# Kernel tuning notes

Measured on AMD Instinct MI355X. Metric: run time of the kernel, lower is better.

Reference implementation:

```python
import jax, jax.numpy as jnp
import numpy as np
import math

B_SZ, L, D_MODEL = 2, 2048, 1024
D_STATE, D_CONV, EXPAND = 16, 4, 2
D_INNER = EXPAND * D_MODEL
DT_RANK = math.ceil(D_MODEL / 16)


def setup_inputs() -> dict:
    key = jax.random.key(0)
    ks = jax.random.split(key, 9)
    s = 0.02
    x = jax.random.normal(ks[0], (B_SZ, L, D_MODEL), jnp.float32)
    W_in = jax.random.normal(ks[1], (D_MODEL, 2 * D_INNER), jnp.float32) * s
    conv_w = jax.random.normal(ks[2], (D_INNER, D_CONV), jnp.float32) * 0.1
    conv_b = jax.random.normal(ks[3], (D_INNER,), jnp.float32) * s
    W_xproj = jax.random.normal(ks[4], (D_INNER, DT_RANK + 2 * D_STATE), jnp.float32) * s
    W_dt = jax.random.normal(ks[5], (DT_RANK, D_INNER), jnp.float32) * s
    # dt bias init so softplus(bias) is log-uniform in [dt_min, dt_max]
    dt_min, dt_max = 0.001, 0.1
    dt = jnp.exp(jax.random.uniform(ks[6], (D_INNER,)) * (math.log(dt_max) - math.log(dt_min)) + math.log(dt_min))
    dt = jnp.maximum(dt, 1e-4)
    b_dt = dt + jnp.log(-jnp.expm1(-dt))
    A_log = jnp.log(jnp.broadcast_to(jnp.arange(1, D_STATE + 1, dtype=jnp.float32), (D_INNER, D_STATE)))
    D = jnp.ones((D_INNER,), jnp.float32)
    W_out = jax.random.normal(ks[7], (D_INNER, D_MODEL), jnp.float32) * s
    return {"x": x, "W_in": W_in, "conv_w": conv_w, "conv_b": conv_b,
            "W_xproj": W_xproj, "W_dt": W_dt, "b_dt": b_dt,
            "A_log": A_log, "D": D, "W_out": W_out}


def _silu(v):
    return v * jax.nn.sigmoid(v)


def _mamba_fwd(x, W_in, conv_w, conv_b, W_xproj, W_dt, b_dt, A_log, D, W_out):
    B, Ls, _ = x.shape
    xz = x @ W_in                         # (B, L, 2*d_inner)
    xb, z = jnp.split(xz, 2, axis=-1)
    # causal depthwise conv1d (pad left d_conv-1, truncate to L)
    xp = jnp.pad(xb, ((0, 0), (D_CONV - 1, 0), (0, 0)))
    conv = conv_b
    acc = jnp.zeros_like(xb)
    for k in range(D_CONV):
        acc = acc + xp[:, k:k + Ls, :] * conv_w[:, k]
    xb = _silu(acc + conv_b)
    # input-dependent dt, B, C
    proj = xb @ W_xproj                   # (B, L, dt_rank + 2*d_state)
    dt_in = proj[..., :DT_RANK]
    Bm = proj[..., DT_RANK:DT_RANK + D_STATE]   # (B, L, d_state)
    Cm = proj[..., DT_RANK + D_STATE:]          # (B, L, d_state)
    dt = jax.nn.softplus(dt_in @ W_dt + b_dt)   # (B, L, d_inner)
    A = -jnp.exp(A_log)                         # (d_inner, d_state)

    def step(h, inp):
        x_t, dt_t, B_t, C_t = inp               # (B,d_inner),(B,d_inner),(B,s),(B,s)
        dA = jnp.exp(dt_t[:, :, None] * A)      # (B, d_inner, d_state)
        h = dA * h + (dt_t[:, :, None] * B_t[:, None, :]) * x_t[:, :, None]
        y_t = jnp.einsum('bds,bs->bd', h, C_t)
        return h, y_t

    h0 = jnp.zeros((B, D_INNER, D_STATE), xb.dtype)
    xs = (xb.swapaxes(0, 1), dt.swapaxes(0, 1), Bm.swapaxes(0, 1), Cm.swapaxes(0, 1))
    _, ys = jax.lax.scan(step, h0, xs)          # (L, B, d_inner)
    y = ys.swapaxes(0, 1) + D * xb
    y = y * _silu(z)
    return y @ W_out                            # (B, L, d_model)


def reference(x, W_in, conv_w, conv_b, W_xproj, W_dt, b_dt, A_log, D, W_out):
    return _mamba_fwd(x, W_in, conv_w, conv_b, W_xproj, W_dt, b_dt, A_log, D, W_out)
```

## Files before the change

### kernel.cpp

```cpp
#include <hip/hip_runtime.h>
#include <hip/hip_bf16.h>
#include <math.h>

#define BSZ 2
#define LSEQ 2048
#define DMODEL 1024
#define DSTATE 16
#define DCONV 4
#define DINNER 2048
#define DTRANK 64
#define NPROJ (DTRANK + 2 * DSTATE)
#define NC 32
#define LC 64
#define KS 4
#define KCH (DINNER / KS)
#define TT 8

using short8 = __attribute__((ext_vector_type(8))) short;
using f32x4 = __attribute__((ext_vector_type(4))) float;
using u16x4 = __attribute__((ext_vector_type(4))) unsigned short;

__device__ __forceinline__ float silu_f(float v) {
    return v / (1.f + expf(-v));
}
__device__ __forceinline__ float softplus_f(float v) {
    return fmaxf(v, 0.f) + log1pf(expf(-fabsf(v)));
}
__device__ __forceinline__ unsigned short f2bf(float f) {
    unsigned u = __builtin_bit_cast(unsigned, f);
    u += 0x7fffu + ((u >> 16) & 1u);
    return (unsigned short)(u >> 16);
}
__device__ __forceinline__ float bf2f(unsigned short u) {
    unsigned x = ((unsigned)u) << 16;
    return __builtin_bit_cast(float, x);
}

__device__ __forceinline__ void gld_lds16(const unsigned short* g, unsigned short* l) {
    __builtin_amdgcn_global_load_lds(
        (const __attribute__((address_space(1))) unsigned int*)g,
        (__attribute__((address_space(3))) unsigned int*)l, 16, 0, 0);
}

__global__ __launch_bounds__(256) void f32_to_bf16_kernel(
    const float* __restrict__ in, unsigned short* __restrict__ out, int n4) {
    int i = blockIdx.x * 256 + threadIdx.x;
    if (i >= n4) return;
    float4 v = reinterpret_cast<const float4*>(in)[i];
    u16x4 o = {f2bf(v.x), f2bf(v.y), f2bf(v.z), f2bf(v.w)};
    reinterpret_cast<u16x4*>(out)[i] = o;
}

__global__ __launch_bounds__(256) void transpose_bf16_kernel(
    const float* __restrict__ in, unsigned short* __restrict__ out, int R, int Cc) {
    __shared__ float t[32][33];
    const int tx = threadIdx.x & 31, ty = threadIdx.x >> 5;
    const int c0 = blockIdx.x * 32, r0 = blockIdx.y * 32;
    for (int i = ty; i < 32; i += 8)
        t[i][tx] = in[(size_t)(r0 + i) * Cc + c0 + tx];
    __syncthreads();
    for (int i = ty; i < 32; i += 8)
        out[(size_t)(c0 + i) * R + r0 + tx] = f2bf(t[tx][i]);
}

template <int EPI, typename CT>
__global__ __launch_bounds__(512) void gemm256(
    const unsigned short* __restrict__ A, const unsigned short* __restrict__ Bt,
    CT* __restrict__ C, CT* __restrict__ C2, int M, int N, int K) {
    extern __shared__ __align__(16) unsigned short lds[];
    unsigned short* As = lds;
    unsigned short* Bs = lds + 3 * 8192;
    const int tid = threadIdx.x;
    const int lane = tid & 63;
    const int w = tid >> 6;
    const int wm = w >> 2, wn = w & 3;
    const int m0 = blockIdx.y * 256, n0 = blockIdx.x * 256;
    const int fr = lane & 15, kg = lane >> 4;
    const int kswz = ((kg ^ ((fr >> 1) & 3)) << 3);
    const int srow = tid >> 2;
    const int cs8 = (((tid & 3) ^ ((tid >> 3) & 3)) << 3);
    const int dst = tid * 8;
    const int nt = K / 32;

    f32x4 acc[8][4];
#pragma unroll
    for (int m = 0; m < 8; m++)
#pragma unroll
        for (int n = 0; n < 4; n++) acc[m][n] = (f32x4){0.f, 0.f, 0.f, 0.f};

#define STAGE_A(t)                                                               \
    {                                                                            \
        const int _b = (t) % 3, _k = (t) * 32;                                   \
        gld_lds16(&A[(size_t)(m0 + srow) * K + _k + cs8], &As[_b * 8192 + dst]); \
        gld_lds16(&A[(size_t)(m0 + 128 + srow) * K + _k + cs8],                  \
                  &As[_b * 8192 + dst + 4096]);                                  \
    }
#define STAGE_B(t)                                                               \
    {                                                                            \
        const int _b = (t) % 3, _k = (t) * 32;                                   \
        gld_lds16(&Bt[(size_t)(n0 + srow) * K + _k + cs8], &Bs[_b * 8192 + dst]);\
        gld_lds16(&Bt[(size_t)(n0 + 128 + srow) * K + _k + cs8],                 \
                  &Bs[_b * 8192 + dst + 4096]);                                  \
    }

    STAGE_A(0); STAGE_B(0); STAGE_A(1); STAGE_B(1);
    asm volatile("s_waitcnt vmcnt(4)" ::: "memory");
    __builtin_amdgcn_s_barrier();

    short8 bfr[4];
    for (int t = 0; t < nt; t++) {
        const int buf = t % 3;
        short8 afr[4];
#pragma unroll
        for (int q = 0; q < 4; q++)
            afr[q] = *reinterpret_cast<const short8*>(
                &As[buf * 8192 + (wm * 128 + q * 16 + fr) * 32 + kswz]);
#pragma unroll
        for (int q = 0; q < 4; q++)
            bfr[q] = *reinterpret_cast<const short8*>(
                &Bs[buf * 8192 + (wn * 64 + q * 16 + fr) * 32 + kswz]);
        if (t + 2 < nt) STAGE_A(t + 2);
        __builtin_amdgcn_s_barrier();
        asm volatile("s_waitcnt lgkmcnt(0)" ::: "memory");
        __builtin_amdgcn_sched_barrier(0);
        __builtin_amdgcn_s_setprio(1);
#pragma unroll
        for (int m = 0; m < 4; m++)
#pragma unroll
            for (int n = 0; n < 4; n++)
                acc[m][n] = __builtin_amdgcn_mfma_f32_16x16x32_bf16(
                    afr[m], bfr[n], acc[m][n], 0, 0, 0);
        __builtin_amdgcn_s_setprio(0);
        __builtin_amdgcn_s_barrier();
#pragma unroll
        for (int q = 0; q < 4; q++)
            afr[q] = *reinterpret_cast<const short8*>(
                &As[buf * 8192 + (wm * 128 + 64 + q * 16 + fr) * 32 + kswz]);
        if (t + 2 < nt) STAGE_B(t + 2);
        if (t + 1 < nt) {
            if (t + 2 < nt)
                asm volatile("s_waitcnt vmcnt(4)" ::: "memory");
            else
                asm volatile("s_waitcnt vmcnt(0)" ::: "memory");
        }
        __builtin_amdgcn_s_barrier();
        asm volatile("s_waitcnt lgkmcnt(0)" ::: "memory");
        __builtin_amdgcn_sched_barrier(0);
        __builtin_amdgcn_s_setprio(1);
#pragma unroll
        for (int m = 0; m < 4; m++)
#pragma unroll
            for (int n = 0; n < 4; n++)
                acc[4 + m][n] = __builtin_amdgcn_mfma_f32_16x16x32_bf16(
                    afr[m], bfr[n], acc[4 + m][n], 0, 0, 0);
        __builtin_amdgcn_s_setprio(0);
        __builtin_amdgcn_s_barrier();
    }
#undef STAGE_A
#undef STAGE_B

    const int g4 = kg * 4;
#pragma unroll
    for (int m = 0; m < 8; m++)
#pragma unroll
        for (int n = 0; n < 4; n++)
#pragma unroll
            for (int j = 0; j < 4; j++) {
                int mm = m0 + wm * 128 + m * 16 + g4 + j;
                int nn = n0 + wn * 64 + n * 16 + fr;
                float v = acc[m][n][j];
                if (EPI == 1) {
                    if (nn < DINNER)
                        C[(size_t)mm * DINNER + nn] = f2bf(v);
                    else
                        C2[(size_t)mm * DINNER + (nn - DINNER)] = f2bf(silu_f(v));
                } else {
                    if constexpr (sizeof(CT) == 2)
                        C[(size_t)mm * N + nn] = f2bf(v);
                    else
                        C[(size_t)mm * N + nn] = v;
                }
            }
}

template <int EPI, int BN, typename CT>
__global__ __launch_bounds__(256) void gemm_mfma(
    const unsigned short* __restrict__ A, const unsigned short* __restrict__ Bt,
    CT* __restrict__ C, CT* __restrict__ C2, const float* __restrict__ bias,
    int M, int N, int K) {
    constexpr int NF = BN / 32;
    __shared__ __align__(16) unsigned short As[2][4096];
    __shared__ __align__(16) unsigned short Bs[2][BN * 32];
    const int tid = threadIdx.x;
    const int lane = tid & 63;
    const int wid = tid >> 6;
    const int wr = wid >> 1, wc = wid & 1;
    const int m0 = blockIdx.y * 128, n0 = blockIdx.x * BN;

    const int r0 = tid >> 2;
    const int r1 = r0 + 64;
    const int d0 = tid * 8;
    const int d1 = d0 + 2048;
    const int cs8 = (((tid & 3) ^ ((tid >> 3) & 3)) << 3);

    f32x4 acc[4][NF];
#pragma unroll
    for (int m = 0; m < 4; m++)
#pragma unroll
        for (int n = 0; n < NF; n++) acc[m][n] = (f32x4){0.f, 0.f, 0.f, 0.f};

    const int fr = lane & 15;
    const int kg = lane >> 4;
    const int kswz = ((kg ^ ((fr >> 1) & 3)) << 3);
    const int nt = K / 32;

    gld_lds16(&A[(size_t)(m0 + r0) * K + cs8], &As[0][d0]);
    gld_lds16(&A[(size_t)(m0 + r1) * K + cs8], &As[0][d1]);
    gld_lds16(&Bt[(size_t)(n0 + r0) * K + cs8], &Bs[0][d0]);
    if constexpr (BN == 128)
        gld_lds16(&Bt[(size_t)(n0 + r1) * K + cs8], &Bs[0][d1]);
    __syncthreads();

    int cur = 0;
    for (int t = 0; t < nt; t++) {
        if (t + 1 < nt) {
            const int k0 = (t + 1) * 32;
            gld_lds16(&A[(size_t)(m0 + r0) * K + k0 + cs8], &As[cur ^ 1][d0]);
            gld_lds16(&A[(size_t)(m0 + r1) * K + k0 + cs8], &As[cur ^ 1][d1]);
            gld_lds16(&Bt[(size_t)(n0 + r0) * K + k0 + cs8], &Bs[cur ^ 1][d0]);
            if constexpr (BN == 128)
                gld_lds16(&Bt[(size_t)(n0 + r1) * K + k0 + cs8], &Bs[cur ^ 1][d1]);
        }
        short8 a[4], b[NF];
#pragma unroll
        for (int m = 0; m < 4; m++)
            a[m] = *reinterpret_cast<const short8*>(
                &As[cur][(wr * 64 + m * 16 + fr) * 32 + kswz]);
#pragma unroll
        for (int n = 0; n < NF; n++)
            b[n] = *reinterpret_cast<const short8*>(
                &Bs[cur][(wc * (BN / 2) + n * 16 + fr) * 32 + kswz]);
#pragma unroll
        for (int m = 0; m < 4; m++)
#pragma unroll
            for (int n = 0; n < NF; n++)
                acc[m][n] = __builtin_amdgcn_mfma_f32_16x16x32_bf16(
                    a[m], b[n], acc[m][n], 0, 0, 0);
        __syncthreads();
        cur ^= 1;
    }

    const int g4 = (lane >> 4) * 4;
#pragma unroll
    for (int m = 0; m < 4; m++)
#pragma unroll
        for (int n = 0; n < NF; n++)
#pragma unroll
            for (int j = 0; j < 4; j++) {
                int mm = m0 + wr * 64 + m * 16 + g4 + j;
                int nn = n0 + wc * (BN / 2) + n * 16 + fr;
                float v = acc[m][n][j];
                if (EPI == 2) v = softplus_f(v + bias[nn]);
                if constexpr (sizeof(CT) == 2)
                    C[(size_t)mm * N + nn] = f2bf(v);
                else
                    C[(size_t)mm * N + nn] = v;
            }
}

__global__ __launch_bounds__(256) void proj_splitk(
    const unsigned short* __restrict__ Abf,
    const unsigned short* __restrict__ WxT,
    float* __restrict__ pp) {
    const int lane = threadIdx.x & 63;
    const int wid = threadIdx.x >> 6;
    const int mt = wid >> 1;
    const int nh = wid & 1;
    const int m0 = blockIdx.x * 32;
    const int kc = blockIdx.y;
    const int fr = lane & 15;
    const int kg = lane >> 4;

    const size_t abase = (size_t)(m0 + mt * 16 + fr) * DINNER + kc * KCH + kg * 8;

    f32x4 acc[3];
#pragma unroll
    for (int i = 0; i < 3; i++) acc[i] = (f32x4){0.f, 0.f, 0.f, 0.f};

    for (int step = 0; step < KCH / 32; step++) {
        short8 a = *reinterpret_cast<const short8*>(&Abf[abase + step * 32]);
#pragma unroll
        for (int nt = 0; nt < 3; nt++) {
            int nrow = nh * 48 + nt * 16 + fr;
            short8 b = *reinterpret_cast<const short8*>(
                &WxT[(size_t)nrow * DINNER + kc * KCH + step * 32 + kg * 8]);
            acc[nt] = __builtin_amdgcn_mfma_f32_16x16x32_bf16(a, b, acc[nt], 0, 0, 0);
        }
    }
    const int g4 = (lane >> 4) * 4;
#pragma unroll
    for (int nt = 0; nt < 3; nt++)
#pragma unroll
        for (int j = 0; j < 4; j++) {
            int m = m0 + mt * 16 + g4 + j;
            int n = nh * 48 + nt * 16 + fr;
            pp[((size_t)kc * (BSZ * LSEQ) + m) * NPROJ + n] = acc[nt][j];
        }
}

__global__ __launch_bounds__(256) void proj_reduce(
    const float* __restrict__ pp, float* __restrict__ proj,
    unsigned short* __restrict__ dtin) {
    int i = blockIdx.x * 256 + threadIdx.x;
    if (i >= BSZ * LSEQ * NPROJ) return;
    float s = 0.f;
#pragma unroll
    for (int kc = 0; kc < KS; kc++)
        s += pp[(size_t)kc * BSZ * LSEQ * NPROJ + i];
    proj[i] = s;
    int m = i / NPROJ;
    int n = i - m * NPROJ;
    if (n < DTRANK) dtin[(size_t)m * DTRANK + n] = f2bf(s);
}

__global__ __launch_bounds__(256) void conv_silu_kernel(
    const unsigned short* __restrict__ xin, const float* __restrict__ w,
    const float* __restrict__ bconv, unsigned short* __restrict__ xout) {
    const int tid = threadIdx.x;
    const int d0 = tid * 8;
    const int bt0 = blockIdx.x * TT;
    const int tloc = bt0 & (LSEQ - 1);

    float wk0[8], wk1[8], wk2[8], wk3[8], bb[8];
#pragma unroll
    for (int q = 0; q < 8; q++) {
        float4 wv = *reinterpret_cast<const float4*>(&w[(d0 + q) * 4]);
        wk0[q] = wv.x; wk1[q] = wv.y; wk2[q] = wv.z; wk3[q] = wv.w;
    }
    {
        float4 b0 = *reinterpret_cast<const float4*>(&bconv[d0]);
        float4 b1 = *reinterpret_cast<const float4*>(&bconv[d0 + 4]);
        bb[0] = b0.x; bb[1] = b0.y; bb[2] = b0.z; bb[3] = b0.w;
        bb[4] = b1.x; bb[5] = b1.y; bb[6] = b1.z; bb[7] = b1.w;
    }

    float xm3[8], xm2[8], xm1[8];
    if (tloc >= 3) {
        short8 v3 = *reinterpret_cast<const short8*>(&xin[(size_t)(bt0 - 3) * DINNER + d0]);
        short8 v2 = *reinterpret_cast<const short8*>(&xin[(size_t)(bt0 - 2) * DINNER + d0]);
        short8 v1 = *reinterpret_cast<const short8*>(&xin[(size_t)(bt0 - 1) * DINNER + d0]);
#pragma unroll
        for (int q = 0; q < 8; q++) {
            xm3[q] = bf2f((unsigned short)v3[q]);
            xm2[q] = bf2f((unsigned short)v2[q]);
            xm1[q] = bf2f((unsigned short)v1[q]);
        }
    } else {
#pragma unroll
        for (int q = 0; q < 8; q++) { xm3[q] = 0.f; xm2[q] = 0.f; xm1[q] = 0.f; }
    }

#pragma unroll
    for (int i = 0; i < TT; i++) {
        short8 vc = *reinterpret_cast<const short8*>(&xin[(size_t)(bt0 + i) * DINNER + d0]);
        float xc[8];
        short8 o;
#pragma unroll
        for (int q = 0; q < 8; q++) {
            xc[q] = bf2f((unsigned short)vc[q]);
            float a = bb[q];
            a = fmaf(wk0[q], xm3[q], a);
            a = fmaf(wk1[q], xm2[q], a);
            a = fmaf(wk2[q], xm1[q], a);
            a = fmaf(wk3[q], xc[q], a);
            o[q] = (short)f2bf(silu_f(a));
        }
        *reinterpret_cast<short8*>(&xout[(size_t)(bt0 + i) * DINNER + d0]) = o;
#pragma unroll
        for (int q = 0; q < 8; q++) { xm3[q] = xm2[q]; xm2[q] = xm1[q]; xm1[q] = xc[q]; }
    }
}

__global__ __launch_bounds__(256) void scan_pass1(
    const unsigned short* __restrict__ xb, const unsigned short* __restrict__ dt,
    const float* __restrict__ proj, const float* __restrict__ A_log,
    float* __restrict__ aprod, float* __restrict__ hend) {
    __shared__ float Bs[LC][DSTATE];
    const int tg = blockIdx.x * 256 + threadIdx.x;
    const int d = tg & (DINNER - 1);
    const int bc = tg >> 11;
    const int c = bc & (NC - 1);
    const int b = bc >> 5;

    for (int idx = threadIdx.x; idx < LC * DSTATE; idx += 256) {
        int ti = idx >> 4, j = idx & 15;
        Bs[ti][j] = proj[(size_t)(b * LSEQ + c * LC + ti) * NPROJ + DTRANK + j];
    }
    __syncthreads();

    float Av[DSTATE], h[DSTATE], ap[DSTATE];
#pragma unroll
    for (int s = 0; s < DSTATE; s++) {
        Av[s] = -expf(A_log[d * DSTATE + s]);
        h[s] = 0.f;
        ap[s] = 1.f;
    }

    for (int i = 0; i < LC; i++) {
        size_t base = (size_t)(b * LSEQ + c * LC + i) * DINNER + d;
        float dtv = bf2f(dt[base]);
        float xv = bf2f(xb[base]);
        float dx = dtv * xv;
#pragma unroll
        for (int s = 0; s < DSTATE; s++) {
            float dA = __expf(dtv * Av[s]);
            ap[s] *= dA;
            h[s] = fmaf(dA, h[s], dx * Bs[i][s]);
        }
    }

    size_t o = ((size_t)bc * DINNER + d) * DSTATE;
#pragma unroll
    for (int q = 0; q < 4; q++) {
        *reinterpret_cast<float4*>(&aprod[o + q * 4]) =
            make_float4(ap[4 * q], ap[4 * q + 1], ap[4 * q + 2], ap[4 * q + 3]);
        *reinterpret_cast<float4*>(&hend[o + q * 4]) =
            make_float4(h[4 * q], h[4 * q + 1], h[4 * q + 2], h[4 * q + 3]);
    }
}

__global__ __launch_bounds__(256) void scan_pass2(
    float* __restrict__ aprod, const float* __restrict__ hend) {
    const int tg = blockIdx.x * 256 + threadIdx.x;
    const int s = tg & (DSTATE - 1);
    const int d = (tg >> 4) & (DINNER - 1);
    const int b = tg >> 15;
    float h = 0.f;
    for (int c = 0; c < NC; c++) {
        size_t o = ((size_t)((b * NC + c) * DINNER) + d) * DSTATE + s;
        float a = aprod[o];
        float e = hend[o];
        aprod[o] = h;
        h = fmaf(a, h, e);
    }
}

__global__ __launch_bounds__(256) void scan_pass3(
    const unsigned short* __restrict__ xb, const unsigned short* __restrict__ dt,
    const float* __restrict__ proj, const float* __restrict__ hstart,
    const float* __restrict__ A_log, const float* __restrict__ Dp,
    const unsigned short* __restrict__ sz, unsigned short* __restrict__ ybf) {
    __shared__ float Bs[LC][DSTATE];
    __shared__ float Cs[LC][DSTATE];
    const int tg = blockIdx.x * 256 + threadIdx.x;
    const int d = tg & (DINNER - 1);
    const int bc = tg >> 11;
    const int c = bc & (NC - 1);
    const int b = bc >> 5;

    for (int idx = threadIdx.x; idx < LC * 2 * DSTATE; idx += 256) {
        int ti = idx >> 5, j = idx & 31;
        float v = proj[(size_t)(b * LSEQ + c * LC + ti) * NPROJ + DTRANK + j];
        if (j < DSTATE) Bs[ti][j] = v;
        else            Cs[ti][j - DSTATE] = v;
    }
    __syncthreads();

    float Av[DSTATE], h[DSTATE];
    size_t o = ((size_t)bc * DINNER + d) * DSTATE;
#pragma unroll
    for (int q = 0; q < 4; q++) {
        float4 hv = *reinterpret_cast<const float4*>(&hstart[o + q * 4]);
        h[4 * q] = hv.x; h[4 * q + 1] = hv.y; h[4 * q + 2] = hv.z; h[4 * q + 3] = hv.w;
    }
#pragma unroll
    for (int s = 0; s < DSTATE; s++)
        Av[s] = -expf(A_log[d * DSTATE + s]);
    const float Dd = Dp[d];

    for (int i = 0; i < LC; i++) {
        size_t base = (size_t)(b * LSEQ + c * LC + i) * DINNER + d;
        float dtv = bf2f(dt[base]);
        float xv = bf2f(xb[base]);
        float szv = bf2f(sz[base]);
        float dx = dtv * xv;
        float p = 0.f;
#pragma unroll
        for (int s = 0; s < DSTATE; s++) {
            float dA = __expf(dtv * Av[s]);
            h[s] = fmaf(dA, h[s], dx * Bs[i][s]);
            p = fmaf(h[s], Cs[i][s], p);
        }
        ybf[base] = f2bf((p + Dd * xv) * szv);
    }
}

extern "C" void kernel_launch(void* const* d_in, const int* in_sizes, int n_in,
                              void* d_out, int out_size, void* d_ws,
                              size_t ws_size, hipStream_t stream) {
    const float* x = (const float*)d_in[0];
    const float* W_in = (const float*)d_in[1];
    const float* conv_w = (const float*)d_in[2];
    const float* conv_b = (const float*)d_in[3];
    const float* W_xproj = (const float*)d_in[4];
    const float* W_dt = (const float*)d_in[5];
    const float* b_dt = (const float*)d_in[6];
    const float* A_log = (const float*)d_in[7];
    const float* Dp = (const float*)d_in[8];
    const float* W_out = (const float*)d_in[9];
    float* out = (float*)d_out;

    char* ws = (char*)d_ws;
    const size_t MB = 1u << 20;
    float* pp    = (float*)(ws);
    float* aprod = (float*)(ws);
    float* hend  = (float*)(ws + 8 * MB);
    unsigned short* xbpre_bf = (unsigned short*)(ws + 16 * MB);
    unsigned short* sz_bf    = (unsigned short*)(ws + 32 * MB);
    unsigned short* xb_bf    = (unsigned short*)(ws + 48 * MB);
    unsigned short* dt_bf    = (unsigned short*)(ws + 64 * MB);
    unsigned short* ybf      = (unsigned short*)(ws + 80 * MB);
    float* projbuf           = (float*)(ws + 88 * MB);
    unsigned short* dtin_bf  = (unsigned short*)(ws + 90 * MB);
    unsigned short* xbf      = (unsigned short*)(ws + 91 * MB);
    unsigned short* WinT     = (unsigned short*)(ws + 99 * MB);
    unsigned short* WoutT    = (unsigned short*)(ws + 107 * MB);
    unsigned short* WxT      = (unsigned short*)(ws + 111 * MB);
    unsigned short* WdtT     = (unsigned short*)(ws + 112 * MB);

    const int M = BSZ * LSEQ;
    dim3 blk(256);

    f32_to_bf16_kernel<<<dim3((M * DMODEL / 4 + 255) / 256), blk, 0, stream>>>(
        x, xbf, M * DMODEL / 4);
    transpose_bf16_kernel<<<dim3(2 * DINNER / 32, DMODEL / 32), blk, 0, stream>>>(
        W_in, WinT, DMODEL, 2 * DINNER);
    transpose_bf16_kernel<<<dim3(DMODEL / 32, DINNER / 32), blk, 0, stream>>>(
        W_out, WoutT, DINNER, DMODEL);
    transpose_bf16_kernel<<<dim3(NPROJ / 32, DINNER / 32), blk, 0, stream>>>(
        W_xproj, WxT, DINNER, NPROJ);
    transpose_bf16_kernel<<<dim3(DINNER / 32, DTRANK / 32), blk, 0, stream>>>(
        W_dt, WdtT, DTRANK, DINNER);

    gemm256<1, unsigned short><<<dim3((2 * DINNER) / 256, M / 256), dim3(512),
                                 98304, stream>>>(
        xbf, WinT, xbpre_bf, sz_bf, M, 2 * DINNER, DMODEL);

    conv_silu_kernel<<<dim3(M / TT), blk, 0, stream>>>(
        xbpre_bf, conv_w, conv_b, xb_bf);

    proj_splitk<<<dim3(M / 32, KS), blk, 0, stream>>>(xb_bf, WxT, pp);
    proj_reduce<<<dim3((M * NPROJ) / 256), blk, 0, stream>>>(pp, projbuf, dtin_bf);

    gemm_mfma<2, 128, unsigned short><<<dim3(DINNER / 128, M / 128), blk, 0, stream>>>(
        dtin_bf, WdtT, dt_bf, nullptr, b_dt, M, DINNER, DTRANK);

    const int nthreads1 = BSZ * NC * DINNER;
    scan_pass1<<<dim3(nthreads1 / 256), blk, 0, stream>>>(
        xb_bf, dt_bf, projbuf, A_log, aprod, hend);
    const int nthreads2 = BSZ * DINNER * DSTATE;
    scan_pass2<<<dim3(nthreads2 / 256), blk, 0, stream>>>(aprod, hend);
    scan_pass3<<<dim3(nthreads1 / 256), blk, 0, stream>>>(
        xb_bf, dt_bf, projbuf, aprod, A_log, Dp, sz_bf, ybf);

    gemm_mfma<0, 128, float><<<dim3(DMODEL / 128, M / 128), blk, 0, stream>>>(
        ybf, WoutT, out, nullptr, nullptr, M, DMODEL, DINNER);
}
```

Before: 274.6 us.

## Add XCD-aware block swizzle and dedicated LDS-free dt projection GEMM

```diff
diff --git a/kernel.cpp b/kernel.cpp
--- a/kernel.cpp
+++ b/kernel.cpp
@@ -42,6 +42,10 @@
         (__attribute__((address_space(3))) unsigned int*)l, 16, 0, 0);
 }
 
+__device__ __forceinline__ int xcd_swz(int wg, int nwg) {
+    return (wg & 7) * (nwg >> 3) + (wg >> 3);
+}
+
 __global__ __launch_bounds__(256) void f32_to_bf16_kernel(
     const float* __restrict__ in, unsigned short* __restrict__ out, int n4) {
     int i = blockIdx.x * 256 + threadIdx.x;
@@ -74,7 +78,9 @@
     const int lane = tid & 63;
     const int w = tid >> 6;
     const int wm = w >> 2, wn = w & 3;
-    const int m0 = blockIdx.y * 256, n0 = blockIdx.x * 256;
+    const int nwg = gridDim.x * gridDim.y;
+    const int wg = xcd_swz(blockIdx.y * gridDim.x + blockIdx.x, nwg);
+    const int m0 = (wg / gridDim.x) * 256, n0 = (wg % gridDim.x) * 256;
     const int fr = lane & 15, kg = lane >> 4;
     const int kswz = ((kg ^ ((fr >> 1) & 3)) << 3);
     const int srow = tid >> 2;
@@ -183,19 +189,19 @@
             }
 }
 
-template <int EPI, int BN, typename CT>
+template <int EPI, typename CT>
 __global__ __launch_bounds__(256) void gemm_mfma(
     const unsigned short* __restrict__ A, const unsigned short* __restrict__ Bt,
-    CT* __restrict__ C, CT* __restrict__ C2, const float* __restrict__ bias,
-    int M, int N, int K) {
-    constexpr int NF = BN / 32;
+    CT* __restrict__ C, int M, int N, int K) {
     __shared__ __align__(16) unsigned short As[2][4096];
-    __shared__ __align__(16) unsigned short Bs[2][BN * 32];
+    __shared__ __align__(16) unsigned short Bs[2][4096];
     const int tid = threadIdx.x;
     const int lane = tid & 63;
     const int wid = tid >> 6;
     const int wr = wid >> 1, wc = wid & 1;
-    const int m0 = blockIdx.y * 128, n0 = blockIdx.x * BN;
+    const int nwg = gridDim.x * gridDim.y;
+    const int wg = xcd_swz(blockIdx.y * gridDim.x + blockIdx.x, nwg);
+    const int m0 = (wg / gridDim.x) * 128, n0 = (wg % gridDim.x) * 128;
 
     const int r0 = tid >> 2;
     const int r1 = r0 + 64;
@@ -203,11 +209,11 @@
     const int d1 = d0 + 2048;
     const int cs8 = (((tid & 3) ^ ((tid >> 3) & 3)) << 3);
 
-    f32x4 acc[4][NF];
+    f32x4 acc[4][4];
 #pragma unroll
     for (int m = 0; m < 4; m++)
 #pragma unroll
-        for (int n = 0; n < NF; n++) acc[m][n] = (f32x4){0.f, 0.f, 0.f, 0.f};
+        for (int n = 0; n < 4; n++) acc[m][n] = (f32x4){0.f, 0.f, 0.f, 0.f};
 
     const int fr = lane & 15;
     const int kg = lane >> 4;
@@ -217,8 +223,7 @@
     gld_lds16(&A[(size_t)(m0 + r0) * K + cs8], &As[0][d0]);
     gld_lds16(&A[(size_t)(m0 + r1) * K + cs8], &As[0][d1]);
     gld_lds16(&Bt[(size_t)(n0 + r0) * K + cs8], &Bs[0][d0]);
-    if constexpr (BN == 128)
-        gld_lds16(&Bt[(size_t)(n0 + r1) * K + cs8], &Bs[0][d1]);
+    gld_lds16(&Bt[(size_t)(n0 + r1) * K + cs8], &Bs[0][d1]);
     __syncthreads();
 
     int cur = 0;
@@ -228,22 +233,21 @@
             gld_lds16(&A[(size_t)(m0 + r0) * K + k0 + cs8], &As[cur ^ 1][d0]);
             gld_lds16(&A[(size_t)(m0 + r1) * K + k0 + cs8], &As[cur ^ 1][d1]);
             gld_lds16(&Bt[(size_t)(n0 + r0) * K + k0 + cs8], &Bs[cur ^ 1][d0]);
-            if constexpr (BN == 128)
-                gld_lds16(&Bt[(size_t)(n0 + r1) * K + k0 + cs8], &Bs[cur ^ 1][d1]);
-        }
-        short8 a[4], b[NF];
+            gld_lds16(&Bt[(size_t)(n0 + r1) * K + k0 + cs8], &Bs[cur ^ 1][d1]);
+        }
+        short8 a[4], b[4];
 #pragma unroll
         for (int m = 0; m < 4; m++)
             a[m] = *reinterpret_cast<const short8*>(
                 &As[cur][(wr * 64 + m * 16 + fr) * 32 + kswz]);
 #pragma unroll
-        for (int n = 0; n < NF; n++)
+        for (int n = 0; n < 4; n++)
             b[n] = *reinterpret_cast<const short8*>(
-                &Bs[cur][(wc * (BN / 2) + n * 16 + fr) * 32 + kswz]);
+                &Bs[cur][(wc * 64 + n * 16 + fr) * 32 + kswz]);
 #pragma unroll
         for (int m = 0; m < 4; m++)
 #pragma unroll
-            for (int n = 0; n < NF; n++)
+            for (int n = 0; n < 4; n++)
                 acc[m][n] = __builtin_amdgcn_mfma_f32_16x16x32_bf16(
                     a[m], b[n], acc[m][n], 0, 0, 0);
         __syncthreads();
@@ -254,18 +258,55 @@
 #pragma unroll
     for (int m = 0; m < 4; m++)
 #pragma unroll
-        for (int n = 0; n < NF; n++)
+        for (int n = 0; n < 4; n++)
 #pragma unroll
             for (int j = 0; j < 4; j++) {
                 int mm = m0 + wr * 64 + m * 16 + g4 + j;
-                int nn = n0 + wc * (BN / 2) + n * 16 + fr;
+                int nn = n0 + wc * 64 + n * 16 + fr;
                 float v = acc[m][n][j];
-                if (EPI == 2) v = softplus_f(v + bias[nn]);
                 if constexpr (sizeof(CT) == 2)
                     C[(size_t)mm * N + nn] = f2bf(v);
                 else
                     C[(size_t)mm * N + nn] = v;
             }
+}
+
+__global__ __launch_bounds__(256) void dt_gemm(
+    const unsigned short* __restrict__ dtin,
+    const unsigned short* __restrict__ WdtT,
+    const float* __restrict__ bias,
+    unsigned short* __restrict__ dtout) {
+    const int lane = threadIdx.x & 63;
+    const int wid = threadIdx.x >> 6;
+    const int mt = wid >> 1, nh = wid & 1;
+    const int m0 = blockIdx.x * 32;
+    const int n0 = blockIdx.y * 128 + nh * 64;
+    const int fr = lane & 15, kg = lane >> 4;
+
+    f32x4 acc[4];
+#pragma unroll
+    for (int i = 0; i < 4; i++) acc[i] = (f32x4){0.f, 0.f, 0.f, 0.f};
+
+#pragma unroll
+    for (int step = 0; step < 2; step++) {
+        short8 a = *reinterpret_cast<const short8*>(
+            &dtin[(size_t)(m0 + mt * 16 + fr) * DTRANK + step * 32 + kg * 8]);
+#pragma unroll
+        for (int nt = 0; nt < 4; nt++) {
+            short8 b = *reinterpret_cast<const short8*>(
+                &WdtT[(size_t)(n0 + nt * 16 + fr) * DTRANK + step * 32 + kg * 8]);
+            acc[nt] = __builtin_amdgcn_mfma_f32_16x16x32_bf16(a, b, acc[nt], 0, 0, 0);
+        }
+    }
+    const int g4 = kg * 4;
+#pragma unroll
+    for (int nt = 0; nt < 4; nt++)
+#pragma unroll
+        for (int j = 0; j < 4; j++) {
+            int m = m0 + mt * 16 + g4 + j;
+            int n = n0 + nt * 16 + fr;
+            dtout[(size_t)m * DINNER + n] = f2bf(softplus_f(acc[nt][j] + bias[n]));
+        }
 }
 
 __global__ __launch_bounds__(256) void proj_splitk(
@@ -516,10 +557,10 @@
     float* aprod = (float*)(ws);
     float* hend  = (float*)(ws + 8 * MB);
     unsigned short* xbpre_bf = (unsigned short*)(ws + 16 * MB);
+    unsigned short* ybf      = (unsigned short*)(ws + 16 * MB);
     unsigned short* sz_bf    = (unsigned short*)(ws + 32 * MB);
     unsigned short* xb_bf    = (unsigned short*)(ws + 48 * MB);
     unsigned short* dt_bf    = (unsigned short*)(ws + 64 * MB);
-    unsigned short* ybf      = (unsigned short*)(ws + 80 * MB);
     float* projbuf           = (float*)(ws + 88 * MB);
     unsigned short* dtin_bf  = (unsigned short*)(ws + 90 * MB);
     unsigned short* xbf      = (unsigned short*)(ws + 91 * MB);
@@ -552,8 +593,8 @@
     proj_splitk<<<dim3(M / 32, KS), blk, 0, stream>>>(xb_bf, WxT, pp);
     proj_reduce<<<dim3((M * NPROJ) / 256), blk, 0, stream>>>(pp, projbuf, dtin_bf);
 
-    gemm_mfma<2, 128, unsigned short><<<dim3(DINNER / 128, M / 128), blk, 0, stream>>>(
-        dtin_bf, WdtT, dt_bf, nullptr, b_dt, M, DINNER, DTRANK);
+    dt_gemm<<<dim3(M / 32, DINNER / 128), blk, 0, stream>>>(
+        dtin_bf, WdtT, b_dt, dt_bf);
 
     const int nthreads1 = BSZ * NC * DINNER;
     scan_pass1<<<dim3(nthreads1 / 256), blk, 0, stream>>>(
@@ -563,6 +604,6 @@
     scan_pass3<<<dim3(nthreads1 / 256), blk, 0, stream>>>(
         xb_bf, dt_bf, projbuf, aprod, A_log, Dp, sz_bf, ybf);
 
-    gemm_mfma<0, 128, float><<<dim3(DMODEL / 128, M / 128), blk, 0, stream>>>(
-        ybf, WoutT, out, nullptr, nullptr, M, DMODEL, DINNER);
-}
+    gemm_mfma<0, float><<<dim3(DMODEL / 128, M / 128), blk, 0, stream>>>(
+        ybf, WoutT, out, M, DMODEL, DINNER);
+}
```

Result: no change. 270.1 us (-1.6%).
